# Kernel optimization log

Hardware: AMD Instinct MI355X
Metric: run time of the kernel (lower is better)

## Reference

```python
import jax, jax.numpy as jnp
import numpy as np

UNITS = 256
IN_DIM = 256
BATCH = 65536


def setup_inputs() -> dict:
    key = jax.random.key(0)
    ks = jax.random.split(key, 5)
    x = jax.random.normal(ks[0], (BATCH, IN_DIM), dtype=jnp.float32)
    h = jax.random.normal(ks[1], (BATCH, UNITS), dtype=jnp.float32)
    c = jax.random.normal(ks[2], (BATCH, UNITS), dtype=jnp.float32)
    kernel = jax.random.normal(ks[3], (IN_DIM, 4 * UNITS), dtype=jnp.float32) * 0.05
    recurrent_kernel = jax.random.normal(ks[4], (UNITS, 4 * UNITS), dtype=jnp.float32) * 0.05
    bias = jnp.zeros((4 * UNITS,), dtype=jnp.float32)
    return {"x": x, "h": h, "c": c, "kernel": kernel,
            "recurrent_kernel": recurrent_kernel, "bias": bias}


def reference(x, h, c, kernel, recurrent_kernel, bias):
    # Fused gate projection: z = x@W + h@U + b, shape [B, 4*units]
    z = x @ kernel + h @ recurrent_kernel + bias
    z_i, z_f, z_g, z_o = jnp.split(z, 4, axis=-1)
    i = jax.nn.sigmoid(z_i)
    f = jax.nn.sigmoid(z_f)
    g = jnp.tanh(z_g)
    o = jax.nn.sigmoid(z_o)
    c_new = f * c + i * g
    h_new = o * jnp.tanh(c_new)
    return h_new, c_new
```

## Files before the change

kernel.cpp:

```cpp
#include <hip/hip_runtime.h>
#include <stdint.h>

#define BATCH   65536
#define BM      128
#define NSTEP   16

typedef __bf16 bf16x8 __attribute__((ext_vector_type(8)));
typedef float  f32x16 __attribute__((ext_vector_type(16)));

__device__ __forceinline__ uint32_t f2bf1(float v) {
  uint32_t u = __float_as_uint(v);
  return (u + 0x7FFFu + ((u >> 16) & 1u)) >> 16;
}

__device__ __forceinline__ float fast_sigmoid(float x) {
  return __builtin_amdgcn_rcpf(1.0f + __expf(-x));
}
__device__ __forceinline__ float fast_tanh(float x) {
  return 1.0f - 2.0f * __builtin_amdgcn_rcpf(1.0f + __expf(2.0f * x));
}

#define WAITVM(N) asm volatile("s_waitcnt vmcnt(" #N ")" ::: "memory")

__global__ __launch_bounds__(256) void prep_weights(
    const float* __restrict__ wk, const float* __restrict__ wr,
    uint4* __restrict__ img) {
  int t  = blockIdx.x * 256 + threadIdx.x;
  int u5 = t & 31;
  int g  = (t >> 5) & 3;
  int kc = (t >> 7) & 3;
  int ks = (t >> 9) & 15;
  int nb = t >> 13;
  int k0  = ks * 32 + kc * 8;
  int col = g * 256 + nb * 32 + u5;
  uint32_t o[4];
#pragma unroll
  for (int p = 0; p < 4; ++p) {
    int k = k0 + p * 2;
    float s0 = (k     < 256) ? wk[(size_t)k * 1024 + col]       : wr[(size_t)(k - 256) * 1024 + col];
    float s1 = (k + 1 < 256) ? wk[(size_t)(k + 1) * 1024 + col] : wr[(size_t)(k - 255) * 1024 + col];
    o[p] = f2bf1(s0) | (f2bf1(s1) << 16);
  }
  img[t] = make_uint4(o[0], o[1], o[2], o[3]);
}

__global__ __launch_bounds__(256) void lstm_fused(
    const float* __restrict__ xp, const float* __restrict__ hp,
    const float* __restrict__ cp, const float* __restrict__ bp,
    const uint4* __restrict__ img, float* __restrict__ outp) {

  __shared__ __align__(16) char smem[32768];

  const int tid  = threadIdx.x;
  const int lane = tid & 63;
  const int wv   = tid >> 6;
  const int ln31 = lane & 31;
  const int hi32 = lane >> 5;

  const int orig = blockIdx.x;
  const int wg   = (orig & 7) * 512 + (orig >> 3);
  const int nb   = wg & 7;
  const int rt   = wg >> 3;

  const int row = rt * BM + wv * 32 + ln31;
  const float* ar = xp + (size_t)row * 256;
  const float* hr = hp + (size_t)row * 256;
  const int koff = hi32 * 8;

  const uint4* bsrc = img + (size_t)nb * 8192 + wv * 128 + lane;

  f32x16 acc[4];
#pragma unroll
  for (int g = 0; g < 4; ++g)
#pragma unroll
    for (int i = 0; i < 16; ++i) acc[g][i] = 0.0f;

  float4 a0[4], a1[4];

  auto loadA = [&](int ks, float4* A) {
    const float* s = ((ks < 8) ? ar : hr) + (ks & 7) * 32 + koff;
    A[0] = *(const float4*)(s);
    A[1] = *(const float4*)(s + 4);
    A[2] = *(const float4*)(s + 16);
    A[3] = *(const float4*)(s + 20);
  };
  auto glds = [&](int ks, int buf) {
    const uint4* src = bsrc + (size_t)ks * 512;
    char* dst = smem + buf * 8192 + wv * 2048;
    __builtin_amdgcn_global_load_lds(
        (const __attribute__((address_space(1))) uint32_t*)src,
        (__attribute__((address_space(3))) uint32_t*)dst, 16, 0, 0);
    __builtin_amdgcn_global_load_lds(
        (const __attribute__((address_space(1))) uint32_t*)(src + 64),
        (__attribute__((address_space(3))) uint32_t*)(dst + 1024), 16, 0, 0);
  };
  auto mkfrag = [&](const float4* A, bf16x8* F) {
#pragma unroll
    for (int h = 0; h < 2; ++h) {
      float4 lo = A[h * 2], hi = A[h * 2 + 1];
      bf16x8 f;
      f[0] = (__bf16)lo.x; f[1] = (__bf16)lo.y; f[2] = (__bf16)lo.z; f[3] = (__bf16)lo.w;
      f[4] = (__bf16)hi.x; f[5] = (__bf16)hi.y; f[6] = (__bf16)hi.z; f[7] = (__bf16)hi.w;
      F[h] = f;
    }
  };
  auto compute = [&](int buf, const bf16x8* F) {
    const char* bb = smem + buf * 8192;
#pragma unroll
    for (int hh = 0; hh < 2; ++hh) {
      const char* bk = bb + (hh * 2 + hi32) * 2048 + ln31 * 16;
#pragma unroll
      for (int g = 0; g < 4; ++g) {
        bf16x8 bfr = *(const bf16x8*)(bk + g * 512);
        acc[g] = __builtin_amdgcn_mfma_f32_32x32x16_bf16(F[hh], bfr, acc[g], 0, 0, 0);
      }
    }
  };

  glds(0, 0);
  glds(1, 1);
  loadA(0, a0);

#pragma unroll
  for (int ks = 0; ks < NSTEP; ++ks) {
    float4* Ac = (ks & 1) ? a1 : a0;
    float4* An = (ks & 1) ? a0 : a1;
    if (ks + 2 < NSTEP) glds(ks + 2, (ks + 2) & 3);
    if (ks + 1 < NSTEP) loadA(ks + 1, An);
    if (ks < NSTEP - 2)      WAITVM(6);
    else if (ks == NSTEP - 2) WAITVM(4);
    else                      WAITVM(0);
    bf16x8 F[2];
    mkfrag(Ac, F);
    __builtin_amdgcn_s_barrier();
    compute(ks & 3, F);
  }

  const int u = nb * 32 + ln31;
  const float bi  = bp[u];
  const float bf_ = bp[256 + u];
  const float bg  = bp[512 + u];
  const float bo  = bp[768 + u];
  const int rowbase = rt * BM + wv * 32 + 4 * hi32;
  float* outh = outp;
  float* outc = outp + (size_t)BATCH * 256;
#pragma unroll
  for (int r = 0; r < 16; ++r) {
    int orow = rowbase + (r & 3) + 8 * (r >> 2);
    size_t idx = (size_t)orow * 256 + u;
    float zi = acc[0][r] + bi;
    float zf = acc[1][r] + bf_;
    float zg = acc[2][r] + bg;
    float zo = acc[3][r] + bo;
    float iv = fast_sigmoid(zi);
    float fv = fast_sigmoid(zf);
    float gv = fast_tanh(zg);
    float ov = fast_sigmoid(zo);
    float cv = __builtin_nontemporal_load(cp + idx);
    float cn = fv * cv + iv * gv;
    float hn = ov * fast_tanh(cn);
    __builtin_nontemporal_store(hn, outh + idx);
    __builtin_nontemporal_store(cn, outc + idx);
  }
}

extern "C" void kernel_launch(void* const* d_in, const int* in_sizes, int n_in,
                              void* d_out, int out_size, void* d_ws, size_t ws_size,
                              hipStream_t stream) {
  const float* x  = (const float*)d_in[0];
  const float* h  = (const float*)d_in[1];
  const float* c  = (const float*)d_in[2];
  const float* wk = (const float*)d_in[3];
  const float* wr = (const float*)d_in[4];
  const float* b  = (const float*)d_in[5];
  prep_weights<<<256, 256, 0, stream>>>(wk, wr, (uint4*)d_ws);
  lstm_fused<<<4096, 256, 0, stream>>>(x, h, c, b,
                                       (const uint4*)d_ws, (float*)d_out);
}
```

Measured before the change: 169.5 us.

## Deepen load pipeline to three stages and prefetch cell state early

Moves from double buffering to triple buffering. Activation loads and global-to-LDS weight loads are now issued three steps ahead, with vmcnt waits adjusted to match. The per-row cell-state and bias loads are issued before the main loop, so their latency hides behind the GEMM instead of stalling the epilogue. The barrier now sits before the next async weight load, and the MFMA section is wrapped in s_setprio. The cost is more registers per thread (an extra A buffer plus 16 cached c values), which may lower occupancy.

```diff
diff --git a/kernel.cpp b/kernel.cpp
--- a/kernel.cpp
+++ b/kernel.cpp
@@ -21,6 +21,7 @@
 }
 
 #define WAITVM(N) asm volatile("s_waitcnt vmcnt(" #N ")" ::: "memory")
+#define MEMF      asm volatile("" ::: "memory")
 
 __global__ __launch_bounds__(256) void prep_weights(
     const float* __restrict__ wk, const float* __restrict__ wr,
@@ -75,7 +76,7 @@
 #pragma unroll
     for (int i = 0; i < 16; ++i) acc[g][i] = 0.0f;
 
-  float4 a0[4], a1[4];
+  float4 a[3][4];
 
   auto loadA = [&](int ks, float4* A) {
     const float* s = ((ks < 8) ? ar : hr) + (ks & 7) * 32 + koff;
@@ -117,31 +118,45 @@
     }
   };
 
-  glds(0, 0);
-  glds(1, 1);
-  loadA(0, a0);
+  const int u = nb * 32 + ln31;
+  const int rowbase = rt * BM + wv * 32 + 4 * hi32;
 
+  glds(0, 0); MEMF;
+  loadA(0, a[0]); MEMF;
+  glds(1, 1); MEMF;
+  loadA(1, a[1]); MEMF;
+  glds(2, 2); MEMF;
+  loadA(2, a[2]); MEMF;
+  float cr[16];
 #pragma unroll
-  for (int ks = 0; ks < NSTEP; ++ks) {
-    float4* Ac = (ks & 1) ? a1 : a0;
-    float4* An = (ks & 1) ? a0 : a1;
-    if (ks + 2 < NSTEP) glds(ks + 2, (ks + 2) & 3);
-    if (ks + 1 < NSTEP) loadA(ks + 1, An);
-    if (ks < NSTEP - 2)      WAITVM(6);
-    else if (ks == NSTEP - 2) WAITVM(4);
-    else                      WAITVM(0);
-    bf16x8 F[2];
-    mkfrag(Ac, F);
-    __builtin_amdgcn_s_barrier();
-    compute(ks & 3, F);
+  for (int r = 0; r < 16; ++r) {
+    int orow = rowbase + (r & 3) + 8 * (r >> 2);
+    cr[r] = __builtin_nontemporal_load(cp + (size_t)orow * 256 + u);
   }
-
-  const int u = nb * 32 + ln31;
+  MEMF;
   const float bi  = bp[u];
   const float bf_ = bp[256 + u];
   const float bg  = bp[512 + u];
   const float bo  = bp[768 + u];
-  const int rowbase = rt * BM + wv * 32 + 4 * hi32;
+  MEMF;
+
+#pragma unroll
+  for (int ks = 0; ks < NSTEP; ++ks) {
+    if (ks < 3)        WAITVM(32);
+    else if (ks < 14)  WAITVM(12);
+    else if (ks == 14) WAITVM(6);
+    else               WAITVM(0);
+    __builtin_amdgcn_s_barrier();
+    MEMF;
+    if (ks + 3 < NSTEP) { glds(ks + 3, (ks + 3) & 3); MEMF; }
+    bf16x8 F[2];
+    mkfrag(a[ks % 3], F);
+    if (ks + 3 < NSTEP) { loadA(ks + 3, a[ks % 3]); MEMF; }
+    __builtin_amdgcn_s_setprio(1);
+    compute(ks & 3, F);
+    __builtin_amdgcn_s_setprio(0);
+  }
+
   float* outh = outp;
   float* outc = outp + (size_t)BATCH * 256;
 #pragma unroll
@@ -156,8 +171,7 @@
     float fv = fast_sigmoid(zf);
     float gv = fast_tanh(zg);
     float ov = fast_sigmoid(zo);
-    float cv = __builtin_nontemporal_load(cp + idx);
-    float cn = fv * cv + iv * gv;
+    float cn = fv * cr[r] + iv * gv;
     float hn = ov * fast_tanh(cn);
     __builtin_nontemporal_store(hn, outh + idx);
     __builtin_nontemporal_store(cn, outc + idx);
```

Measured after the change: 168.1 us. Within noise of the previous version (-0.9%).

## Load weight fragments directly into registers instead of staging through LDS

Applied to the files above, without the earlier changes.

Removes the shared-memory staging of the bf16 weight tiles and the per-step block barrier. Each wave now loads its own B fragments from global memory (L2-resident) into a double-buffered register set, and the A prefetch is deepened to three stages. MFMA sections are wrapped in s_setprio, and launch bounds request two blocks per CU. The cost is higher register pressure and four times more redundant global/L2 reads of the weights, since every wave fetches the same B data.

```diff
diff --git a/kernel.cpp b/kernel.cpp
--- a/kernel.cpp
+++ b/kernel.cpp
@@ -19,8 +19,6 @@
 __device__ __forceinline__ float fast_tanh(float x) {
   return 1.0f - 2.0f * __builtin_amdgcn_rcpf(1.0f + __expf(2.0f * x));
 }
-
-#define WAITVM(N) asm volatile("s_waitcnt vmcnt(" #N ")" ::: "memory")
 
 __global__ __launch_bounds__(256) void prep_weights(
     const float* __restrict__ wk, const float* __restrict__ wr,
@@ -44,12 +42,10 @@
   img[t] = make_uint4(o[0], o[1], o[2], o[3]);
 }
 
-__global__ __launch_bounds__(256) void lstm_fused(
+__global__ __launch_bounds__(256, 2) void lstm_fused(
     const float* __restrict__ xp, const float* __restrict__ hp,
     const float* __restrict__ cp, const float* __restrict__ bp,
     const uint4* __restrict__ img, float* __restrict__ outp) {
-
-  __shared__ __align__(16) char smem[32768];
 
   const int tid  = threadIdx.x;
   const int lane = tid & 63;
@@ -67,7 +63,7 @@
   const float* hr = hp + (size_t)row * 256;
   const int koff = hi32 * 8;
 
-  const uint4* bsrc = img + (size_t)nb * 8192 + wv * 128 + lane;
+  const uint4* bsrc = img + (size_t)nb * 8192 + hi32 * 128 + ln31;
 
   f32x16 acc[4];
 #pragma unroll
@@ -75,7 +71,8 @@
 #pragma unroll
     for (int i = 0; i < 16; ++i) acc[g][i] = 0.0f;
 
-  float4 a0[4], a1[4];
+  float4 a[3][4];
+  uint4  b[2][8];
 
   auto loadA = [&](int ks, float4* A) {
     const float* s = ((ks < 8) ? ar : hr) + (ks & 7) * 32 + koff;
@@ -84,15 +81,13 @@
     A[2] = *(const float4*)(s + 16);
     A[3] = *(const float4*)(s + 20);
   };
-  auto glds = [&](int ks, int buf) {
-    const uint4* src = bsrc + (size_t)ks * 512;
-    char* dst = smem + buf * 8192 + wv * 2048;
-    __builtin_amdgcn_global_load_lds(
-        (const __attribute__((address_space(1))) uint32_t*)src,
-        (__attribute__((address_space(3))) uint32_t*)dst, 16, 0, 0);
-    __builtin_amdgcn_global_load_lds(
-        (const __attribute__((address_space(1))) uint32_t*)(src + 64),
-        (__attribute__((address_space(3))) uint32_t*)(dst + 1024), 16, 0, 0);
+  auto loadB = [&](int ks, uint4* B) {
+    const uint4* s = bsrc + (size_t)ks * 512;
+#pragma unroll
+    for (int hh = 0; hh < 2; ++hh)
+#pragma unroll
+      for (int g = 0; g < 4; ++g)
+        B[hh * 4 + g] = s[hh * 256 + g * 32];
   };
   auto mkfrag = [&](const float4* A, bf16x8* F) {
 #pragma unroll
@@ -104,36 +99,28 @@
       F[h] = f;
     }
   };
-  auto compute = [&](int buf, const bf16x8* F) {
-    const char* bb = smem + buf * 8192;
-#pragma unroll
-    for (int hh = 0; hh < 2; ++hh) {
-      const char* bk = bb + (hh * 2 + hi32) * 2048 + ln31 * 16;
-#pragma unroll
-      for (int g = 0; g < 4; ++g) {
-        bf16x8 bfr = *(const bf16x8*)(bk + g * 512);
-        acc[g] = __builtin_amdgcn_mfma_f32_32x32x16_bf16(F[hh], bfr, acc[g], 0, 0, 0);
-      }
-    }
-  };
 
-  glds(0, 0);
-  glds(1, 1);
-  loadA(0, a0);
+  loadA(0, a[0]);
+  loadB(0, b[0]);
+  loadA(1, a[1]);
+  loadB(1, b[1]);
+  loadA(2, a[2]);
 
 #pragma unroll
   for (int ks = 0; ks < NSTEP; ++ks) {
-    float4* Ac = (ks & 1) ? a1 : a0;
-    float4* An = (ks & 1) ? a0 : a1;
-    if (ks + 2 < NSTEP) glds(ks + 2, (ks + 2) & 3);
-    if (ks + 1 < NSTEP) loadA(ks + 1, An);
-    if (ks < NSTEP - 2)      WAITVM(6);
-    else if (ks == NSTEP - 2) WAITVM(4);
-    else                      WAITVM(0);
     bf16x8 F[2];
-    mkfrag(Ac, F);
-    __builtin_amdgcn_s_barrier();
-    compute(ks & 3, F);
+    mkfrag(a[ks % 3], F);
+    if (ks + 3 < NSTEP) loadA(ks + 3, a[ks % 3]);
+    __builtin_amdgcn_s_setprio(1);
+#pragma unroll
+    for (int hh = 0; hh < 2; ++hh)
+#pragma unroll
+      for (int g = 0; g < 4; ++g) {
+        bf16x8 bfr = __builtin_bit_cast(bf16x8, b[ks & 1][hh * 4 + g]);
+        acc[g] = __builtin_amdgcn_mfma_f32_32x32x16_bf16(F[hh], bfr, acc[g], 0, 0, 0);
+      }
+    __builtin_amdgcn_s_setprio(0);
+    if (ks + 2 < NSTEP) loadB(ks + 2, b[ks & 1]);
   }
 
   const int u = nb * 32 + ln31;
```

After: 230.6 us. 1.36x slower.
